# Optimization experiments

Measured on AMD Instinct MI355X. Metric: run time of the kernel, lower is better.

## Reference

```python
import jax, jax.numpy as jnp
import numpy as np

B, S, D, Fd, M, H, L = 4, 1024, 1024, 4096, 512, 16, 2
HD = D // H
EPS = 1e-5


def _ln(x, s, b):
    m = jnp.mean(x, axis=-1, keepdims=True)
    v = jnp.mean((x - m) ** 2, axis=-1, keepdims=True)
    return (x - m) * jax.lax.rsqrt(v + EPS) * s + b


def _mha(x, Wq, bq, Wk, bk, Wv, bv, Wo, bo):
    b_, s_, _ = x.shape
    Q = (x @ Wq + bq).reshape(b_, s_, H, HD)
    K = (x @ Wk + bk).reshape(b_, s_, H, HD)
    V = (x @ Wv + bv).reshape(b_, s_, H, HD)
    scores = jnp.einsum('bihd,bjhd->bhij', Q, K) / np.sqrt(HD).astype(np.float32)
    w = jax.nn.softmax(scores, axis=-1)
    out = jnp.einsum('bhij,bjhd->bihd', w, V).reshape(b_, s_, D)
    return out @ Wo + bo


def setup_inputs() -> dict:
    key = jax.random.key(0)
    ks = iter(jax.random.split(key, 40))
    w = lambda shape: jax.random.normal(next(ks), shape, jnp.float32) * 0.02
    inp = {
        'x': jax.random.normal(next(ks), (B, S, D), jnp.float32),
        # stacked per-global-layer params [L, ...]
        'Wq': w((L, D, D)), 'bq': jnp.zeros((L, D)),
        'Wk': w((L, D, D)), 'bk': jnp.zeros((L, D)),
        'Wv': w((L, D, D)), 'bv': jnp.zeros((L, D)),
        'Wo': w((L, D, D)), 'bo': jnp.zeros((L, D)),
        'W1': w((L, D, Fd)), 'b1': jnp.zeros((L, Fd)),
        'W2': w((L, Fd, D)), 'b2': jnp.zeros((L, D)),
        'n1s': jnp.ones((L, D)), 'n1b': jnp.zeros((L, D)),
        'n2s': jnp.ones((L, D)), 'n2b': jnp.zeros((L, D)),
        # top-level params
        'ln1s': jnp.ones((D,)), 'ln1b': jnp.zeros((D,)),
        'ln2s': jnp.ones((D,)), 'ln2b': jnp.zeros((D,)),
        'ln3s': jnp.ones((D,)), 'ln3b': jnp.zeros((D,)),
        'Wb': w((D, M)), 'bb': jnp.zeros((M,)),      # backbone stand-in
        'Wm': w((M, D)), 'bm': jnp.zeros((D,)),      # self.linear
        'Wf1': w((D, Fd)), 'bf1': jnp.zeros((Fd,)),  # top feed_forward
        'Wf2': w((Fd, D)), 'bf2': jnp.zeros((D,)),
    }
    return inp


def reference(x, Wq, bq, Wk, bk, Wv, bv, Wo, bo, W1, b1, W2, b2,
              n1s, n1b, n2s, n2b, ln1s, ln1b, ln2s, ln2b, ln3s, ln3b,
              Wb, bb, Wm, bm, Wf1, bf1, Wf2, bf2):
    # dropout is identity (eval mode)
    # global branch: stacked EncoderLayers
    g = x
    for i in range(L):
        a = _mha(g, Wq[i], bq[i], Wk[i], bk[i], Wv[i], bv[i], Wo[i], bo[i])
        g = _ln(g + a, n1s[i], n1b[i])
        ff = jax.nn.relu(g @ W1[i] + b1[i]) @ W2[i] + b2[i]
        g = _ln(g + ff, n2s[i], n2b[i])

    def local(frac):
        st = S // frac
        xs = x[:, -st:, :]
        mo = (xs @ Wb + bb) @ Wm + bm
        y = _ln(xs + mo, ln1s, ln1b)
        return jnp.pad(y, ((0, 0), (S - st, 0), (0, 0)))

    output = g + local(2) + local(4)  # S >= 4 branch
    h = _ln(output + x, ln2s, ln2b)
    ff = jax.nn.relu(output @ Wf1 + bf1) @ Wf2 + bf2
    return _ln(h + ff, ln3s, ln3b)
```

## Files before the change

kernel.cpp:

```cpp
#include <hip/hip_runtime.h>
#include <stdint.h>


typedef short   s16x8 __attribute__((ext_vector_type(8)));
typedef float   f32x4 __attribute__((ext_vector_type(4)));
typedef uint16_t u16x8 __attribute__((ext_vector_type(8)));
typedef uint16_t u16x4 __attribute__((ext_vector_type(4)));

__device__ __forceinline__ float bf2f(uint16_t h) {
    union { uint32_t u; float f; } c; c.u = ((uint32_t)h) << 16; return c.f;
}
__device__ __forceinline__ uint16_t f2bf(float f) {
    union { float f; uint32_t u; } c; c.f = f;
    uint32_t u = c.u;
    u += 0x7fffu + ((u >> 16) & 1u);
    return (uint16_t)(u >> 16);
}

__device__ __forceinline__ void g2l16(const uint16_t* g, uint16_t* l) {
    __builtin_amdgcn_global_load_lds(
        (const __attribute__((address_space(1))) void*)g,
        (__attribute__((address_space(3))) void*)l, 16, 0, 0);
}

template<int MODE, int BN, int BK>
__global__ __launch_bounds__(256) void gemm_bt(
    const uint16_t* __restrict__ A, const uint16_t* __restrict__ Bt,
    const float* __restrict__ bias0, const float* __restrict__ bias1,
    const float* __restrict__ bias2,
    uint16_t* __restrict__ C0, uint16_t* __restrict__ C1,
    uint16_t* __restrict__ C2,
    int M, int N, int K)
{
    constexpr int JN  = BN / 32;
    constexpr int KS  = BK / 32;
    constexpr int CPR = BK / 8;
    constexpr int LG  = (BK == 32) ? 2 : 3;
    constexpr int RA  = (128 * BK / 8) / 256;
    constexpr int RB  = (BN  * BK / 8) / 256;
    __shared__ __align__(16) uint16_t sA[128 * BK];
    __shared__ __align__(16) uint16_t sB[BN * BK];

    const int t    = threadIdx.x;
    const int w    = t >> 6;
    const int lane = t & 63;
    const int qd   = lane >> 4;
    const int cc   = lane & 15;

    int bm, bn;
    {
        int gx = gridDim.x, gy = gridDim.y;
        if ((gy & 7) == 0) {
            int id   = blockIdx.y * gx + blockIdx.x;
            int gpg  = gy >> 3;
            int rest = id >> 3;
            bm = (id & 7) * gpg + rest % gpg;
            bn = rest / gpg;
        } else { bm = blockIdx.y; bn = blockIdx.x; }
    }
    const int m0 = bm * 128;
    const int n0 = bn * BN;
    const int wm = (w >> 1) * 64;
    const int wn = (w & 1) * (BN / 2);

    auto key = [](int row) -> int {
        return (BK == 32) ? ((row >> 1) & 3) : (row & 7);
    };

    f32x4 acc[4][JN];
#pragma unroll
    for (int i = 0; i < 4; ++i)
#pragma unroll
        for (int j = 0; j < JN; ++j) acc[i][j] = (f32x4)0.0f;

    int rA[RA], kA[RA];
#pragma unroll
    for (int is = 0; is < RA; ++is) {
        int gc = is * 256 + t;
        int row = gc >> LG, ph = gc & (CPR - 1);
        rA[is] = row;
        kA[is] = (ph ^ key(row)) * 8;
    }
    int rB[RB], kB[RB];
#pragma unroll
    for (int is = 0; is < RB; ++is) {
        int gc = is * 256 + t;
        int row = gc >> LG, ph = gc & (CPR - 1);
        rB[is] = row;
        kB[is] = (ph ^ key(row)) * 8;
    }
    int offA[4][KS], offB[JN][KS];
#pragma unroll
    for (int i = 0; i < 4; ++i) {
        int ml = wm + i * 16 + cc;
#pragma unroll
        for (int ks = 0; ks < KS; ++ks)
            offA[i][ks] = ml * BK + ((ks * 4 + qd) ^ key(ml)) * 8;
    }
#pragma unroll
    for (int j = 0; j < JN; ++j) {
        int nl = wn + j * 16 + cc;
#pragma unroll
        for (int ks = 0; ks < KS; ++ks)
            offB[j][ks] = nl * BK + ((ks * 4 + qd) ^ key(nl)) * 8;
    }

    for (int kt = 0; kt < K; kt += BK) {
#pragma unroll
        for (int is = 0; is < RA; ++is)
            g2l16(A + (size_t)(m0 + rA[is]) * K + kt + kA[is],
                  sA + (size_t)(is * 256 + w * 64) * 8);
#pragma unroll
        for (int is = 0; is < RB; ++is)
            g2l16(Bt + (size_t)(n0 + rB[is]) * K + kt + kB[is],
                  sB + (size_t)(is * 256 + w * 64) * 8);
        __syncthreads();
#pragma unroll
        for (int ks = 0; ks < KS; ++ks) {
            s16x8 af[4], bv[JN];
#pragma unroll
            for (int i = 0; i < 4; ++i) af[i] = *(const s16x8*)(sA + offA[i][ks]);
#pragma unroll
            for (int j = 0; j < JN; ++j) bv[j] = *(const s16x8*)(sB + offB[j][ks]);
#pragma unroll
            for (int i = 0; i < 4; ++i)
#pragma unroll
                for (int j = 0; j < JN; ++j)
                    acc[i][j] = __builtin_amdgcn_mfma_f32_16x16x32_bf16(
                        af[i], bv[j], acc[i][j], 0, 0, 0);
        }
        __syncthreads();
    }

#pragma unroll
    for (int j = 0; j < JN; ++j) {
        int col = n0 + wn + j * 16 + cc;
        float bb;
        if (MODE == 3) {
            int seg = col >> 10;
            const float* bp = (seg == 0) ? bias0 : (seg == 1) ? bias1 : bias2;
            bb = bp[col & 1023];
        } else {
            bb = bias0[col];
        }
#pragma unroll
        for (int i = 0; i < 4; ++i) {
            f32x4 v = acc[i][j];
#pragma unroll
            for (int r = 0; r < 4; ++r) {
                float val = v[r] + bb;
                if (MODE == 1) val = fmaxf(val, 0.0f);
                int row = m0 + wm + i * 16 + qd * 4 + r;
                if (MODE == 3) {
                    if (col < 1024) {
                        C0[(size_t)row * 1024 + col] = f2bf(val);
                    } else if (col < 2048) {
                        C1[(size_t)row * 1024 + (col - 1024)] = f2bf(val);
                    } else {
                        int c = col - 2048;
                        int b = row >> 10, s = row & 1023;
                        int hh = c >> 6, d = c & 63;
                        C2[((size_t)(b * 16 + hh) * 64 + d) * 1024 + s] = f2bf(val);
                    }
                } else {
                    C0[(size_t)row * N + col] = f2bf(val);
                }
            }
        }
    }
}

#define FA_P 76
__global__ __launch_bounds__(256) void flash_attn(
    const uint16_t* __restrict__ Q, const uint16_t* __restrict__ K,
    const uint16_t* __restrict__ Vt, uint16_t* __restrict__ O)
{
    __shared__ __align__(16) uint16_t Qs[64 * FA_P];
    __shared__ __align__(16) uint16_t Ks[64 * FA_P];
    __shared__ __align__(16) uint16_t Vs[64 * FA_P];
    __shared__ __align__(16) uint16_t Ps[64 * FA_P];

    const int t    = threadIdx.x;
    const int w    = t >> 6;
    const int lane = t & 63;
    const int qd   = lane >> 4;
    const int cc   = lane & 15;
    const int id   = blockIdx.x;
    const int xg   = id & 7;
    const int loc  = id >> 3;
    const int bh   = xg * 8 + (loc >> 4);
    const int qblk = loc & 15;
    const int b    = bh >> 4, hh = bh & 15;
    const size_t rowbase = (size_t)b * 1024;

#pragma unroll
    for (int is = 0; is < 2; ++is) {
        int c = is * 256 + t, r = c >> 3, ch = c & 7;
        *(u16x8*)(Qs + r * FA_P + ch * 8) =
            *(const u16x8*)(Q + (rowbase + qblk * 64 + r) * 1024 + hh * 64 + ch * 8);
    }

    f32x4 o[4];
    float lrow[4] = {0.0f, 0.0f, 0.0f, 0.0f};
#pragma unroll
    for (int j = 0; j < 4; ++j) o[j] = (f32x4)0.0f;

    for (int kb = 0; kb < 1024; kb += 64) {
        __syncthreads();
#pragma unroll
        for (int is = 0; is < 2; ++is) {
            int c = is * 256 + t, r = c >> 3, ch = c & 7;
            *(u16x8*)(Ks + r * FA_P + ch * 8) =
                *(const u16x8*)(K + (rowbase + kb + r) * 1024 + hh * 64 + ch * 8);
            *(u16x8*)(Vs + r * FA_P + ch * 8) =
                *(const u16x8*)(Vt + ((size_t)(bh * 64 + r)) * 1024 + kb + ch * 8);
        }
        __syncthreads();

        f32x4 sc[4];
        s16x8 aq0 = *(const s16x8*)(Qs + (w * 16 + cc) * FA_P + qd * 8);
        s16x8 aq1 = *(const s16x8*)(Qs + (w * 16 + cc) * FA_P + 32 + qd * 8);
#pragma unroll
        for (int j = 0; j < 4; ++j) {
            s16x8 b0 = *(const s16x8*)(Ks + (j * 16 + cc) * FA_P + qd * 8);
            s16x8 b1 = *(const s16x8*)(Ks + (j * 16 + cc) * FA_P + 32 + qd * 8);
            sc[j] = __builtin_amdgcn_mfma_f32_16x16x32_bf16(aq0, b0, (f32x4)0.0f, 0, 0, 0);
            sc[j] = __builtin_amdgcn_mfma_f32_16x16x32_bf16(aq1, b1, sc[j], 0, 0, 0);
        }

#pragma unroll
        for (int r = 0; r < 4; ++r) {
            float p0 = __expf(sc[0][r] * 0.125f);
            float p1 = __expf(sc[1][r] * 0.125f);
            float p2 = __expf(sc[2][r] * 0.125f);
            float p3 = __expf(sc[3][r] * 0.125f);
            lrow[r] += (p0 + p1) + (p2 + p3);
            int prow = (w * 16 + qd * 4 + r) * FA_P + cc;
            Ps[prow]      = f2bf(p0);
            Ps[prow + 16] = f2bf(p1);
            Ps[prow + 32] = f2bf(p2);
            Ps[prow + 48] = f2bf(p3);
        }

#pragma unroll
        for (int ks = 0; ks < 2; ++ks) {
            s16x8 ap = *(const s16x8*)(Ps + (w * 16 + cc) * FA_P + ks * 32 + qd * 8);
#pragma unroll
            for (int j = 0; j < 4; ++j) {
                s16x8 bb = *(const s16x8*)(Vs + (j * 16 + cc) * FA_P + ks * 32 + qd * 8);
                o[j] = __builtin_amdgcn_mfma_f32_16x16x32_bf16(ap, bb, o[j], 0, 0, 0);
            }
        }
    }

#pragma unroll
    for (int r = 0; r < 4; ++r) {
        float rs = lrow[r];
        rs += __shfl_xor(rs, 1);
        rs += __shfl_xor(rs, 2);
        rs += __shfl_xor(rs, 4);
        rs += __shfl_xor(rs, 8);
        float inv = 1.0f / rs;
        size_t grow = rowbase + qblk * 64 + w * 16 + qd * 4 + r;
#pragma unroll
        for (int j = 0; j < 4; ++j)
            O[grow * 1024 + hh * 64 + j * 16 + cc] = f2bf(o[j][r] * inv);
    }
}

template<int BT, int F32OUT>
__global__ __launch_bounds__(256) void ln_res(
    const uint16_t* __restrict__ A, const void* __restrict__ Bp,
    const float* __restrict__ S, const float* __restrict__ Bi,
    void* __restrict__ outp)
{
    const int row = blockIdx.x, t = threadIdx.x;
    const int w = t >> 6, lane = t & 63;
    u16x4 a4 = *(const u16x4*)(A + (size_t)row * 1024 + t * 4);
    float bvals[4];
    if (BT == 0) {
        u16x4 b4 = *(const u16x4*)((const uint16_t*)Bp + (size_t)row * 1024 + t * 4);
#pragma unroll
        for (int e = 0; e < 4; ++e) bvals[e] = bf2f(b4[e]);
    } else {
        float4 b4 = *(const float4*)((const float*)Bp + (size_t)row * 1024 + t * 4);
        bvals[0] = b4.x; bvals[1] = b4.y; bvals[2] = b4.z; bvals[3] = b4.w;
    }
    float v[4], sum = 0.0f, sq = 0.0f;
#pragma unroll
    for (int e = 0; e < 4; ++e) {
        v[e] = bf2f(a4[e]) + bvals[e];
        sum += v[e];
        sq  += v[e] * v[e];
    }
#pragma unroll
    for (int d = 1; d < 64; d <<= 1) {
        sum += __shfl_xor(sum, d);
        sq  += __shfl_xor(sq, d);
    }
    __shared__ float rs[4], rq[4];
    if (lane == 0) { rs[w] = sum; rq[w] = sq; }
    __syncthreads();
    sum = rs[0] + rs[1] + rs[2] + rs[3];
    sq  = rq[0] + rq[1] + rq[2] + rq[3];
    float mean = sum * (1.0f / 1024.0f);
    float var  = sq * (1.0f / 1024.0f) - mean * mean;
    float rstd = rsqrtf(var + 1e-5f);
    float4 s4  = *(const float4*)(S + t * 4);
    float4 bi4 = *(const float4*)(Bi + t * 4);
    float r0 = (v[0] - mean) * rstd * s4.x + bi4.x;
    float r1 = (v[1] - mean) * rstd * s4.y + bi4.y;
    float r2 = (v[2] - mean) * rstd * s4.z + bi4.z;
    float r3 = (v[3] - mean) * rstd * s4.w + bi4.w;
    if (F32OUT) {
        *(float4*)((float*)outp + (size_t)row * 1024 + t * 4) =
            make_float4(r0, r1, r2, r3);
    } else {
        u16x4 o4;
        o4[0] = f2bf(r0); o4[1] = f2bf(r1); o4[2] = f2bf(r2); o4[3] = f2bf(r3);
        *(u16x4*)((uint16_t*)outp + (size_t)row * 1024 + t * 4) = o4;
    }
}

__global__ __launch_bounds__(256) void add3(
    const uint16_t* __restrict__ g, const uint16_t* __restrict__ y2,
    const uint16_t* __restrict__ y4, uint16_t* __restrict__ out)
{
    size_t e = ((size_t)blockIdx.x * 256 + threadIdx.x) * 4;
    int row = (int)(e >> 10), col = (int)(e & 1023);
    int b = row >> 10, s = row & 1023;
    u16x4 gv = *(const u16x4*)(g + e);
    float v[4];
#pragma unroll
    for (int k = 0; k < 4; ++k) v[k] = bf2f(gv[k]);
    if (s >= 512) {
        u16x4 a = *(const u16x4*)(y2 + ((size_t)(b * 512 + s - 512)) * 1024 + col);
#pragma unroll
        for (int k = 0; k < 4; ++k) v[k] += bf2f(a[k]);
    }
    if (s >= 768) {
        u16x4 a = *(const u16x4*)(y4 + ((size_t)(b * 256 + s - 768)) * 1024 + col);
#pragma unroll
        for (int k = 0; k < 4; ++k) v[k] += bf2f(a[k]);
    }
    u16x4 o4;
#pragma unroll
    for (int k = 0; k < 4; ++k) o4[k] = f2bf(v[k]);
    *(u16x4*)(out + e) = o4;
}

__global__ __launch_bounds__(256) void copy_rows_f32(
    const float* __restrict__ x, uint16_t* __restrict__ out, int lgst)
{
    size_t e = ((size_t)blockIdx.x * 256 + threadIdx.x) * 4;
    int row = (int)(e >> 10), col = (int)(e & 1023);
    int st = 1 << lgst;
    int b = row >> lgst, s = row & (st - 1);
    float4 a = *(const float4*)(x + ((size_t)(b * 1024 + (1024 - st) + s)) * 1024 + col);
    u16x4 o4;
    o4[0] = f2bf(a.x); o4[1] = f2bf(a.y); o4[2] = f2bf(a.z); o4[3] = f2bf(a.w);
    *(u16x4*)(out + e) = o4;
}

__global__ __launch_bounds__(256) void transpose_k(
    const float* __restrict__ W, uint16_t* __restrict__ Wt, int Kd, int Nd)
{
    __shared__ uint16_t tile[32][33];
    int tx = threadIdx.x & 31, ty = threadIdx.x >> 5;
    int n0 = blockIdx.x * 32, k0 = blockIdx.y * 32;
#pragma unroll
    for (int j = 0; j < 32; j += 8)
        tile[ty + j][tx] = f2bf(W[(size_t)(k0 + ty + j) * Nd + n0 + tx]);
    __syncthreads();
#pragma unroll
    for (int j = 0; j < 32; j += 8)
        Wt[(size_t)(n0 + ty + j) * Kd + k0 + tx] = tile[tx][ty + j];
}

__global__ __launch_bounds__(256) void cvt(
    const float* __restrict__ src, uint16_t* __restrict__ dst)
{
    size_t i = ((size_t)blockIdx.x * 256 + threadIdx.x) * 8;
    float4 a = *(const float4*)(src + i);
    float4 b = *(const float4*)(src + i + 4);
    u16x8 o;
    o[0] = f2bf(a.x); o[1] = f2bf(a.y); o[2] = f2bf(a.z); o[3] = f2bf(a.w);
    o[4] = f2bf(b.x); o[5] = f2bf(b.y); o[6] = f2bf(b.z); o[7] = f2bf(b.w);
    *(u16x8*)(dst + i) = o;
}

extern "C" void kernel_launch(void* const* d_in, const int* in_sizes, int n_in,
                              void* d_out, int out_size, void* d_ws, size_t ws_size,
                              hipStream_t stream)
{
    const float* x    = (const float*)d_in[0];
    const float* Wq   = (const float*)d_in[1];
    const float* bq   = (const float*)d_in[2];
    const float* Wk   = (const float*)d_in[3];
    const float* bk   = (const float*)d_in[4];
    const float* Wv   = (const float*)d_in[5];
    const float* bv   = (const float*)d_in[6];
    const float* Wo   = (const float*)d_in[7];
    const float* bo   = (const float*)d_in[8];
    const float* W1   = (const float*)d_in[9];
    const float* b1   = (const float*)d_in[10];
    const float* W2   = (const float*)d_in[11];
    const float* b2   = (const float*)d_in[12];
    const float* n1s  = (const float*)d_in[13];
    const float* n1b  = (const float*)d_in[14];
    const float* n2s  = (const float*)d_in[15];
    const float* n2b  = (const float*)d_in[16];
    const float* ln1s = (const float*)d_in[17];
    const float* ln1b = (const float*)d_in[18];
    const float* ln2s = (const float*)d_in[19];
    const float* ln2b = (const float*)d_in[20];
    const float* ln3s = (const float*)d_in[21];
    const float* ln3b = (const float*)d_in[22];
    const float* Wb   = (const float*)d_in[23];
    const float* bb   = (const float*)d_in[24];
    const float* Wm   = (const float*)d_in[25];
    const float* bm   = (const float*)d_in[26];
    const float* Wf1  = (const float*)d_in[27];
    const float* bf1  = (const float*)d_in[28];
    const float* Wf2  = (const float*)d_in[29];
    const float* bf2  = (const float*)d_in[30];

    char* ws = (char*)d_ws;
    const size_t MB = (size_t)1 << 20;
    uint16_t* g    = (uint16_t*)(ws);
    uint16_t* tb   = (uint16_t*)(ws + 8 * MB);
    char*     big  = ws + 16 * MB;
    uint16_t* qb   = (uint16_t*)(big);
    uint16_t* kbuf = (uint16_t*)(big + 8 * MB);
    uint16_t* vtb  = (uint16_t*)(big + 16 * MB);
    uint16_t* ob   = (uint16_t*)(big + 24 * MB);
    uint16_t* ffb  = (uint16_t*)(big);
    uint16_t* xbf  = (uint16_t*)(ws + 48 * MB);
    uint16_t* hb   = (uint16_t*)(ws + 48 * MB);
    uint16_t* wT   = (uint16_t*)(ws + 56 * MB);

    auto T = [&](const float* Wsrc, int Kd, int Nd, uint16_t* dst) {
        transpose_k<<<dim3(Nd / 32, Kd / 32), 256, 0, stream>>>(Wsrc, dst, Kd, Nd);
    };

    cvt<<<2048, 256, 0, stream>>>(x, xbf);

    const uint16_t* gin = xbf;
    for (int i = 0; i < 2; ++i) {
        const size_t wOff = (size_t)i * 1024 * 1024;
        const size_t fOff = (size_t)i * 1024 * 4096;
        T(Wq + wOff, 1024, 1024, wT);
        T(Wk + wOff, 1024, 1024, wT + (size_t)1024 * 1024);
        T(Wv + wOff, 1024, 1024, wT + (size_t)2048 * 1024);
        gemm_bt<3, 128, 32><<<dim3(24, 32), 256, 0, stream>>>(
            gin, wT, bq + i * 1024, bk + i * 1024, bv + i * 1024,
            qb, kbuf, vtb, 4096, 3072, 1024);
        flash_attn<<<1024, 256, 0, stream>>>(qb, kbuf, vtb, ob);
        T(Wo + wOff, 1024, 1024, wT);
        gemm_bt<0, 64, 64><<<dim3(16, 32), 256, 0, stream>>>(
            ob, wT, bo + i * 1024, nullptr, nullptr, tb, nullptr, nullptr,
            4096, 1024, 1024);
        ln_res<0, 0><<<4096, 256, 0, stream>>>(gin, tb, n1s + i * 1024, n1b + i * 1024, g);
        T(W1 + fOff, 1024, 4096, wT);
        gemm_bt<1, 128, 32><<<dim3(32, 32), 256, 0, stream>>>(
            g, wT, b1 + i * 4096, nullptr, nullptr, ffb, nullptr, nullptr,
            4096, 4096, 1024);
        T(W2 + fOff, 4096, 1024, wT);
        gemm_bt<0, 64, 64><<<dim3(16, 32), 256, 0, stream>>>(
            ffb, wT, b2 + i * 1024, nullptr, nullptr, tb, nullptr, nullptr,
            4096, 1024, 4096);
        ln_res<0, 0><<<4096, 256, 0, stream>>>(g, tb, n2s + i * 1024, n2b + i * 1024, g);
        gin = g;
    }

    uint16_t* xsc = (uint16_t*)(big);
    uint16_t* lk  = (uint16_t*)(big + 8 * MB);
    uint16_t* mo  = (uint16_t*)(big + 16 * MB);
    uint16_t* yy  = (uint16_t*)(big + 24 * MB);
    copy_rows_f32<<<2048, 256, 0, stream>>>(x, xsc, 9);
    copy_rows_f32<<<1024, 256, 0, stream>>>(x, xsc + (size_t)2048 * 1024, 8);
    uint16_t* WbT = wT;
    uint16_t* WmT = wT + (size_t)512 * 1024;
    T(Wb, 1024, 512, WbT);
    T(Wm, 512, 1024, WmT);
    gemm_bt<0, 64, 64><<<dim3(8, 24), 256, 0, stream>>>(
        xsc, WbT, bb, nullptr, nullptr, lk, nullptr, nullptr, 3072, 512, 1024);
    gemm_bt<0, 64, 64><<<dim3(16, 24), 256, 0, stream>>>(
        lk, WmT, bm, nullptr, nullptr, mo, nullptr, nullptr, 3072, 1024, 512);
    ln_res<0, 0><<<3072, 256, 0, stream>>>(xsc, mo, ln1s, ln1b, yy);
    uint16_t* y2 = yy;
    uint16_t* y4 = yy + (size_t)2048 * 1024;

    add3<<<4096, 256, 0, stream>>>(g, y2, y4, g);
    ln_res<1, 0><<<4096, 256, 0, stream>>>(g, x, ln2s, ln2b, hb);
    T(Wf1, 1024, 4096, wT);
    gemm_bt<1, 128, 32><<<dim3(32, 32), 256, 0, stream>>>(
        g, wT, bf1, nullptr, nullptr, ffb, nullptr, nullptr, 4096, 4096, 1024);
    T(Wf2, 4096, 1024, wT);
    gemm_bt<0, 64, 64><<<dim3(16, 32), 256, 0, stream>>>(
        ffb, wT, bf2, nullptr, nullptr, tb, nullptr, nullptr, 4096, 1024, 4096);
    ln_res<0, 1><<<4096, 256, 0, stream>>>(hb, tb, ln3s, ln3b, d_out);
}
```

Baseline: 885.0 us.

## Double-buffer LDS in N=64 GEMMs and widen weight transpose tiles

Adds a DB template flag to the GEMM that keeps two LDS buffers, so the next K-tile's global-to-LDS load is issued before computing the current one, with one barrier per iteration instead of two. It is enabled only for the 64x64 tile configurations (Wo, W2, local and Wf2 GEMMs). The weight transpose kernel now uses 64x64 tiles with float4 loads and 16-byte stores to cut launch count and raise memory efficiency. The risks are that double buffering doubles LDS use, which can lower occupancy, and that the transposed LDS writes are narrow and may hit bank conflicts.

```diff
diff --git a/kernel.cpp b/kernel.cpp
--- a/kernel.cpp
+++ b/kernel.cpp
@@ -23,7 +23,7 @@
         (__attribute__((address_space(3))) void*)l, 16, 0, 0);
 }
 
-template<int MODE, int BN, int BK>
+template<int MODE, int BN, int BK, int DB>
 __global__ __launch_bounds__(256) void gemm_bt(
     const uint16_t* __restrict__ A, const uint16_t* __restrict__ Bt,
     const float* __restrict__ bias0, const float* __restrict__ bias1,
@@ -32,14 +32,15 @@
     uint16_t* __restrict__ C2,
     int M, int N, int K)
 {
-    constexpr int JN  = BN / 32;
-    constexpr int KS  = BK / 32;
-    constexpr int CPR = BK / 8;
-    constexpr int LG  = (BK == 32) ? 2 : 3;
-    constexpr int RA  = (128 * BK / 8) / 256;
-    constexpr int RB  = (BN  * BK / 8) / 256;
-    __shared__ __align__(16) uint16_t sA[128 * BK];
-    __shared__ __align__(16) uint16_t sB[BN * BK];
+    constexpr int JN   = BN / 32;
+    constexpr int KS   = BK / 32;
+    constexpr int CPR  = BK / 8;
+    constexpr int LG   = (BK == 32) ? 2 : 3;
+    constexpr int RA   = (128 * BK / 8) / 256;
+    constexpr int RB   = (BN  * BK / 8) / 256;
+    constexpr int NBUF = DB ? 2 : 1;
+    __shared__ __align__(16) uint16_t sA[NBUF][128 * BK];
+    __shared__ __align__(16) uint16_t sB[NBUF][BN * BK];
 
     const int t    = threadIdx.x;
     const int w    = t >> 6;
@@ -105,23 +106,26 @@
             offB[j][ks] = nl * BK + ((ks * 4 + qd) ^ key(nl)) * 8;
     }
 
-    for (int kt = 0; kt < K; kt += BK) {
+    auto stage = [&](int kt, int buf) {
 #pragma unroll
         for (int is = 0; is < RA; ++is)
             g2l16(A + (size_t)(m0 + rA[is]) * K + kt + kA[is],
-                  sA + (size_t)(is * 256 + w * 64) * 8);
+                  sA[buf] + (size_t)(is * 256 + w * 64) * 8);
 #pragma unroll
         for (int is = 0; is < RB; ++is)
             g2l16(Bt + (size_t)(n0 + rB[is]) * K + kt + kB[is],
-                  sB + (size_t)(is * 256 + w * 64) * 8);
-        __syncthreads();
+                  sB[buf] + (size_t)(is * 256 + w * 64) * 8);
+    };
+    auto compute = [&](int buf) {
 #pragma unroll
         for (int ks = 0; ks < KS; ++ks) {
             s16x8 af[4], bv[JN];
 #pragma unroll
-            for (int i = 0; i < 4; ++i) af[i] = *(const s16x8*)(sA + offA[i][ks]);
-#pragma unroll
-            for (int j = 0; j < JN; ++j) bv[j] = *(const s16x8*)(sB + offB[j][ks]);
+            for (int i = 0; i < 4; ++i)
+                af[i] = *(const s16x8*)(sA[buf] + offA[i][ks]);
+#pragma unroll
+            for (int j = 0; j < JN; ++j)
+                bv[j] = *(const s16x8*)(sB[buf] + offB[j][ks]);
 #pragma unroll
             for (int i = 0; i < 4; ++i)
 #pragma unroll
@@ -129,7 +133,25 @@
                     acc[i][j] = __builtin_amdgcn_mfma_f32_16x16x32_bf16(
                         af[i], bv[j], acc[i][j], 0, 0, 0);
         }
+    };
+
+    if (DB) {
+        stage(0, 0);
         __syncthreads();
+        int cur = 0;
+        for (int kt = 0; kt < K; kt += BK) {
+            if (kt + BK < K) stage(kt + BK, cur ^ 1);
+            compute(cur);
+            __syncthreads();
+            cur ^= 1;
+        }
+    } else {
+        for (int kt = 0; kt < K; kt += BK) {
+            stage(kt, 0);
+            __syncthreads();
+            compute(0);
+            __syncthreads();
+        }
     }
 
 #pragma unroll
@@ -365,16 +387,27 @@
 __global__ __launch_bounds__(256) void transpose_k(
     const float* __restrict__ W, uint16_t* __restrict__ Wt, int Kd, int Nd)
 {
-    __shared__ uint16_t tile[32][33];
-    int tx = threadIdx.x & 31, ty = threadIdx.x >> 5;
-    int n0 = blockIdx.x * 32, k0 = blockIdx.y * 32;
-#pragma unroll
-    for (int j = 0; j < 32; j += 8)
-        tile[ty + j][tx] = f2bf(W[(size_t)(k0 + ty + j) * Nd + n0 + tx]);
+    __shared__ uint16_t tile[64][68];
+    const int t  = threadIdx.x;
+    const int n0 = blockIdx.x * 64, k0 = blockIdx.y * 64;
+#pragma unroll
+    for (int p = 0; p < 4; ++p) {
+        int k  = p * 16 + (t >> 4);
+        int nn = (t & 15) * 4;
+        float4 a = *(const float4*)(W + (size_t)(k0 + k) * Nd + n0 + nn);
+        tile[nn + 0][k] = f2bf(a.x);
+        tile[nn + 1][k] = f2bf(a.y);
+        tile[nn + 2][k] = f2bf(a.z);
+        tile[nn + 3][k] = f2bf(a.w);
+    }
     __syncthreads();
 #pragma unroll
-    for (int j = 0; j < 32; j += 8)
-        Wt[(size_t)(n0 + ty + j) * Kd + k0 + tx] = tile[tx][ty + j];
+    for (int p = 0; p < 2; ++p) {
+        int nn = p * 32 + (t >> 3);
+        int kk = (t & 7) * 8;
+        u16x8 o = *(const u16x8*)(&tile[nn][kk]);
+        *(u16x8*)(Wt + (size_t)(n0 + nn) * Kd + k0 + kk) = o;
+    }
 }
 
 __global__ __launch_bounds__(256) void cvt(
@@ -440,7 +473,7 @@
     uint16_t* wT   = (uint16_t*)(ws + 56 * MB);
 
     auto T = [&](const float* Wsrc, int Kd, int Nd, uint16_t* dst) {
-        transpose_k<<<dim3(Nd / 32, Kd / 32), 256, 0, stream>>>(Wsrc, dst, Kd, Nd);
+        transpose_k<<<dim3(Nd / 64, Kd / 64), 256, 0, stream>>>(Wsrc, dst, Kd, Nd);
     };
 
     cvt<<<2048, 256, 0, stream>>>(x, xbf);
@@ -452,21 +485,21 @@
         T(Wq + wOff, 1024, 1024, wT);
         T(Wk + wOff, 1024, 1024, wT + (size_t)1024 * 1024);
         T(Wv + wOff, 1024, 1024, wT + (size_t)2048 * 1024);
-        gemm_bt<3, 128, 32><<<dim3(24, 32), 256, 0, stream>>>(
+        gemm_bt<3, 128, 32, 0><<<dim3(24, 32), 256, 0, stream>>>(
             gin, wT, bq + i * 1024, bk + i * 1024, bv + i * 1024,
             qb, kbuf, vtb, 4096, 3072, 1024);
         flash_attn<<<1024, 256, 0, stream>>>(qb, kbuf, vtb, ob);
         T(Wo + wOff, 1024, 1024, wT);
-        gemm_bt<0, 64, 64><<<dim3(16, 32), 256, 0, stream>>>(
+        gemm_bt<0, 64, 64, 1><<<dim3(16, 32), 256, 0, stream>>>(
             ob, wT, bo + i * 1024, nullptr, nullptr, tb, nullptr, nullptr,
             4096, 1024, 1024);
         ln_res<0, 0><<<4096, 256, 0, stream>>>(gin, tb, n1s + i * 1024, n1b + i * 1024, g);
         T(W1 + fOff, 1024, 4096, wT);
-        gemm_bt<1, 128, 32><<<dim3(32, 32), 256, 0, stream>>>(
+        gemm_bt<1, 128, 32, 0><<<dim3(32, 32), 256, 0, stream>>>(
             g, wT, b1 + i * 4096, nullptr, nullptr, ffb, nullptr, nullptr,
             4096, 4096, 1024);
         T(W2 + fOff, 4096, 1024, wT);
-        gemm_bt<0, 64, 64><<<dim3(16, 32), 256, 0, stream>>>(
+        gemm_bt<0, 64, 64, 1><<<dim3(16, 32), 256, 0, stream>>>(
             ffb, wT, b2 + i * 1024, nullptr, nullptr, tb, nullptr, nullptr,
             4096, 1024, 4096);
         ln_res<0, 0><<<4096, 256, 0, stream>>>(g, tb, n2s + i * 1024, n2b + i * 1024, g);
@@ -483,9 +516,9 @@
     uint16_t* WmT = wT + (size_t)512 * 1024;
     T(Wb, 1024, 512, WbT);
     T(Wm, 512, 1024, WmT);
-    gemm_bt<0, 64, 64><<<dim3(8, 24), 256, 0, stream>>>(
+    gemm_bt<0, 64, 64, 1><<<dim3(8, 24), 256, 0, stream>>>(
         xsc, WbT, bb, nullptr, nullptr, lk, nullptr, nullptr, 3072, 512, 1024);
-    gemm_bt<0, 64, 64><<<dim3(16, 24), 256, 0, stream>>>(
+    gemm_bt<0, 64, 64, 1><<<dim3(16, 24), 256, 0, stream>>>(
         lk, WmT, bm, nullptr, nullptr, mo, nullptr, nullptr, 3072, 1024, 512);
     ln_res<0, 0><<<3072, 256, 0, stream>>>(xsc, mo, ln1s, ln1b, yy);
     uint16_t* y2 = yy;
@@ -494,10 +527,10 @@
     add3<<<4096, 256, 0, stream>>>(g, y2, y4, g);
     ln_res<1, 0><<<4096, 256, 0, stream>>>(g, x, ln2s, ln2b, hb);
     T(Wf1, 1024, 4096, wT);
-    gemm_bt<1, 128, 32><<<dim3(32, 32), 256, 0, stream>>>(
+    gemm_bt<1, 128, 32, 0><<<dim3(32, 32), 256, 0, stream>>>(
         g, wT, bf1, nullptr, nullptr, ffb, nullptr, nullptr, 4096, 4096, 1024);
     T(Wf2, 4096, 1024, wT);
-    gemm_bt<0, 64, 64><<<dim3(16, 32), 256, 0, stream>>>(
+    gemm_bt<0, 64, 64, 1><<<dim3(16, 32), 256, 0, stream>>>(
         ffb, wT, bf2, nullptr, nullptr, tb, nullptr, nullptr, 4096, 1024, 4096);
     ln_res<0, 1><<<4096, 256, 0, stream>>>(hb, tb, ln3s, ln3b, d_out);
 }
```

After: 873.6 us. Within noise of the previous version (-1.3%).
